# Kernel tuning notes

Hardware: AMD Instinct MI355X
Metric: run time of the kernel (lower is better)

The kernel has to match this reference:

```python
import jax, jax.numpy as jnp
import numpy as np

SEQ_LEN, BATCH, HID, ATT = 2048, 64, 512, 512


def setup_inputs() -> dict:
    key = jax.random.key(0)
    k1, k2, k3, k4, k5, k6 = jax.random.split(key, 6)
    return {
        "dec_out": jax.random.normal(k1, (BATCH, HID), dtype=jnp.float32),
        "enc_outs": jax.random.normal(k2, (SEQ_LEN, BATCH, HID), dtype=jnp.float32),
        "W_s": jax.random.normal(k3, (ATT, HID), dtype=jnp.float32) * (1.0 / np.sqrt(HID)),
        "W_t": jax.random.normal(k4, (ATT, HID), dtype=jnp.float32) * (1.0 / np.sqrt(HID)),
        "b_t": jax.random.normal(k5, (ATT,), dtype=jnp.float32) * 0.01,
        "v_a": jax.random.uniform(k6, (ATT,), dtype=jnp.float32, minval=-0.05, maxval=0.05),
    }


def reference(dec_out, enc_outs, W_s, W_t, b_t, v_a):
    # enc_att: (seq_len, batch, att) = W_s @ enc_outs
    enc_att = jnp.einsum('sbh,ah->sba', enc_outs, W_s)
    # dec_att: (batch, att) = W_t @ dec_out + b_t
    dec_att = dec_out @ W_t.T + b_t
    # score(b, s) = v_a . tanh(enc_att[s,b] + dec_att[b])
    scores = jnp.einsum('sba,a->bs', jnp.tanh(enc_att + dec_att[None, :, :]), v_a)
    return scores  # (batch, seq_len)
```

## Files before the change

kernel.cpp:

```cpp
#include <hip/hip_runtime.h>

typedef __attribute__((ext_vector_type(8))) short short8;
typedef __attribute__((ext_vector_type(4))) float f32x4;

#define SEQ 2048
#define BATCH 64
#define HID 512
#define ATT 512

__device__ __forceinline__ unsigned short f2bf(float f) {
  unsigned u = __float_as_uint(f);
  u += 0x7fffu + ((u >> 16) & 1u);
  return (unsigned short)(u >> 16);
}

__device__ __forceinline__ void dma16(const void* g, void* l) {
  __builtin_amdgcn_global_load_lds(
      (const __attribute__((address_space(1))) unsigned int*)g,
      (__attribute__((address_space(3))) unsigned int*)l, 16, 0, 0);
}

__global__ void bahdanau_pre(const float* __restrict__ dec_out,
                             const float* __restrict__ W_t,
                             const float* __restrict__ b_t,
                             const float* __restrict__ W_s,
                             unsigned short* __restrict__ wsb,
                             float* __restrict__ decT) {
  if (blockIdx.x < 64) {
    const int b = blockIdx.x;
    __shared__ float drow[HID];
    for (int i = threadIdx.x; i < HID; i += 256) drow[i] = dec_out[b * HID + i];
    __syncthreads();
    for (int a = threadIdx.x; a < ATT; a += 256) {
      const float4* wr = (const float4*)(W_t + (size_t)a * HID);
      float s0 = 0.f, s1 = 0.f, s2 = 0.f, s3 = 0.f;
#pragma unroll 4
      for (int j = 0; j < HID / 4; ++j) {
        float4 w = wr[j];
        s0 = fmaf(w.x, drow[4 * j + 0], s0);
        s1 = fmaf(w.y, drow[4 * j + 1], s1);
        s2 = fmaf(w.z, drow[4 * j + 2], s2);
        s3 = fmaf(w.w, drow[4 * j + 3], s3);
      }
      decT[a * BATCH + b] = (s0 + s1) + (s2 + s3) + b_t[a];
    }
  } else {
    const int cb = blockIdx.x - 64;
    const float4* src = (const float4*)W_s;
#pragma unroll
    for (int i = 0; i < 4; ++i) {
      int idx = cb * 1024 + i * 256 + threadIdx.x;
      float4 v = src[idx];
      int a = idx >> 7;
      int h = (idx & 127) * 4;
      ushort4 o;
      o.x = f2bf(v.x); o.y = f2bf(v.y); o.z = f2bf(v.z); o.w = f2bf(v.w);
      int blk = (a >> 4) * 64 + ((h >> 3) & 3) * 16 + (a & 15);
      int dst = (h >> 5) * 16384 + blk * 8 + (h & 7);
      *(ushort4*)&wsb[dst] = o;
    }
  }
}

__global__ __launch_bounds__(512, 2)
void bahdanau_main(const float* __restrict__ enc,
                   const unsigned short* __restrict__ wsb,
                   const float* __restrict__ decT,
                   const float* __restrict__ v_a,
                   float* __restrict__ out) {
  __shared__ __align__(16) unsigned char smem[81920];
  unsigned short* Bb[2] = { (unsigned short*)smem, (unsigned short*)(smem + 32768) };
  float* Ab[2] = { (float*)(smem + 65536), (float*)(smem + 73728) };
  float* partial = (float*)(smem + 65536);

  const int tid  = threadIdx.x;
  const int w    = tid >> 6;
  const int lane = tid & 63;
  const int c = lane & 15;
  const int q = lane >> 4;
  const int s = blockIdx.x;
  const int n0 = w * 64;

  const char* encB = (const char*)(enc + (size_t)s * 64 * HID);
  const char* wsbB = (const char*)wsb;

  const int am = (w & 3) * 16 + (lane & 15);
  const int ag = (lane >> 4) * 2 + (w >> 2);
  const char* aSrc = encB + am * 2048 + ag * 16;

  f32x4 acc[4][4];
#pragma unroll
  for (int nt = 0; nt < 4; ++nt)
#pragma unroll
    for (int mt = 0; mt < 4; ++mt)
      acc[mt][nt] = *(const f32x4*)(decT + (size_t)(n0 + nt * 16 + c) * 64 + mt * 16 + q * 4);

  float va[4];
#pragma unroll
  for (int nt = 0; nt < 4; ++nt) va[nt] = v_a[n0 + nt * 16 + c];

  dma16(aSrc, (char*)Ab[0] + w * 1024);
#pragma unroll
  for (int d = 0; d < 4; ++d)
    dma16(wsbB + w * 4096 + d * 1024 + lane * 16, (char*)Bb[0] + w * 4096 + d * 1024);

#pragma unroll
  for (int kb = 0; kb < 16; ++kb) {
    const int cur = kb & 1;
    __syncthreads();

    if (kb < 15) {
      const int nb = kb + 1;
      const int nxt = nb & 1;
      dma16(aSrc + nb * 128, (char*)Ab[nxt] + w * 1024);
#pragma unroll
      for (int d = 0; d < 4; ++d)
        dma16(wsbB + nb * 32768 + w * 4096 + d * 1024 + lane * 16,
              (char*)Bb[nxt] + w * 4096 + d * 1024);
    }

    const float* Ac = Ab[cur];
    const unsigned short* Bc = Bb[cur];
    short8 af[4];
#pragma unroll
    for (int mt = 0; mt < 4; ++mt) {
      float4 lo = *(const float4*)(Ac + (mt * 64 + q * 16 + c) * 4);
      float4 hi = *(const float4*)(Ac + (256 + mt * 64 + q * 16 + c) * 4);
      short8 t;
      t[0] = (short)f2bf(lo.x); t[1] = (short)f2bf(lo.y);
      t[2] = (short)f2bf(lo.z); t[3] = (short)f2bf(lo.w);
      t[4] = (short)f2bf(hi.x); t[5] = (short)f2bf(hi.y);
      t[6] = (short)f2bf(hi.z); t[7] = (short)f2bf(hi.w);
      af[mt] = t;
    }
    short8 bf[4];
#pragma unroll
    for (int nt = 0; nt < 4; ++nt)
      bf[nt] = *(const short8*)(Bc + (((w * 4 + nt) * 64 + q * 16 + c) * 8));

#pragma unroll
    for (int mt = 0; mt < 4; ++mt)
#pragma unroll
      for (int nt = 0; nt < 4; ++nt)
        acc[mt][nt] = __builtin_amdgcn_mfma_f32_16x16x32_bf16(af[mt], bf[nt], acc[mt][nt], 0, 0, 0);
  }

  float rowsum[4][4];
#pragma unroll
  for (int mt = 0; mt < 4; ++mt) {
#pragma unroll
    for (int r = 0; r < 4; ++r) {
      float sum = 0.f;
#pragma unroll
      for (int nt = 0; nt < 4; ++nt) {
        float x = acc[mt][nt][r];
        float e = __builtin_amdgcn_exp2f(x * 2.8853900817779268f);
        float t = 1.f - 2.f * __builtin_amdgcn_rcpf(e + 1.f);
        sum = fmaf(va[nt], t, sum);
      }
      rowsum[mt][r] = sum;
    }
  }

#pragma unroll
  for (int off = 1; off < 16; off <<= 1) {
#pragma unroll
    for (int mt = 0; mt < 4; ++mt)
#pragma unroll
      for (int r = 0; r < 4; ++r)
        rowsum[mt][r] += __shfl_xor(rowsum[mt][r], off, 64);
  }

  if (c == 0) {
#pragma unroll
    for (int mt = 0; mt < 4; ++mt)
#pragma unroll
      for (int r = 0; r < 4; ++r)
        partial[w * 64 + mt * 16 + q * 4 + r] = rowsum[mt][r];
  }
  __syncthreads();

  if (tid < 64) {
    float sum = 0.f;
#pragma unroll
    for (int ww = 0; ww < 8; ++ww) sum += partial[ww * 64 + tid];
    out[(size_t)tid * SEQ + s] = sum;
  }
}

extern "C" void kernel_launch(void* const* d_in, const int* in_sizes, int n_in,
                              void* d_out, int out_size, void* d_ws, size_t ws_size,
                              hipStream_t stream) {
  const float* dec_out = (const float*)d_in[0];
  const float* enc     = (const float*)d_in[1];
  const float* W_s     = (const float*)d_in[2];
  const float* W_t     = (const float*)d_in[3];
  const float* b_t     = (const float*)d_in[4];
  const float* v_a     = (const float*)d_in[5];
  float* out = (float*)d_out;

  unsigned short* wsb = (unsigned short*)d_ws;
  float* decT = (float*)((char*)d_ws + (size_t)ATT * HID * 2);

  bahdanau_pre<<<128, 256, 0, stream>>>(dec_out, W_t, b_t, W_s, wsb, decT);
  bahdanau_main<<<SEQ, 512, 0, stream>>>(enc, wsb, decT, v_a, out);
}
```

Baseline: 489.4 us.

## Load W_s fragments directly to registers and deepen A-tile pipeline

```diff
diff --git a/kernel.cpp b/kernel.cpp
--- a/kernel.cpp
+++ b/kernel.cpp
@@ -19,6 +19,23 @@
       (const __attribute__((address_space(1))) unsigned int*)g,
       (__attribute__((address_space(3))) unsigned int*)l, 16, 0, 0);
 }
+
+__device__ __forceinline__ short8 cvt8(float4 lo, float4 hi) {
+  union { unsigned u[4]; short8 s; } r;
+  asm("v_cvt_pk_bf16_f32 %0, %1, %2" : "=v"(r.u[0]) : "v"(lo.x), "v"(lo.y));
+  asm("v_cvt_pk_bf16_f32 %0, %1, %2" : "=v"(r.u[1]) : "v"(lo.z), "v"(lo.w));
+  asm("v_cvt_pk_bf16_f32 %0, %1, %2" : "=v"(r.u[2]) : "v"(hi.x), "v"(hi.y));
+  asm("v_cvt_pk_bf16_f32 %0, %1, %2" : "=v"(r.u[3]) : "v"(hi.z), "v"(hi.w));
+  return r.s;
+}
+
+#define GLOADS(dst, voff, base, OFF) \
+  asm volatile("global_load_dwordx4 %0, %1, %2 offset:" #OFF \
+               : "=v"(dst) : "v"(voff), "s"(base))
+
+#define BWAIT(N, b0, b1, b2, b3) \
+  asm volatile("s_waitcnt vmcnt(" #N ")" \
+               : "+v"(b0), "+v"(b1), "+v"(b2), "+v"(b3) :: "memory")
 
 __global__ void bahdanau_pre(const float* __restrict__ dec_out,
                              const float* __restrict__ W_t,
@@ -62,16 +79,14 @@
   }
 }
 
-__global__ __launch_bounds__(512, 2)
+__global__ __launch_bounds__(512, 4)
 void bahdanau_main(const float* __restrict__ enc,
                    const unsigned short* __restrict__ wsb,
                    const float* __restrict__ decT,
                    const float* __restrict__ v_a,
                    float* __restrict__ out) {
-  __shared__ __align__(16) unsigned char smem[81920];
-  unsigned short* Bb[2] = { (unsigned short*)smem, (unsigned short*)(smem + 32768) };
-  float* Ab[2] = { (float*)(smem + 65536), (float*)(smem + 73728) };
-  float* partial = (float*)(smem + 65536);
+  __shared__ __align__(16) float Asm[4][2048];
+  __shared__ float partial[512];
 
   const int tid  = threadIdx.x;
   const int w    = tid >> 6;
@@ -82,11 +97,12 @@
   const int n0 = w * 64;
 
   const char* encB = (const char*)(enc + (size_t)s * 64 * HID);
-  const char* wsbB = (const char*)wsb;
-
-  const int am = (w & 3) * 16 + (lane & 15);
-  const int ag = (lane >> 4) * 2 + (w >> 2);
+
+  const int am = (w & 3) * 16 + c;
+  const int ag = q * 2 + (w >> 2);
   const char* aSrc = encB + am * 2048 + ag * 16;
+
+  const unsigned voff = (unsigned)(w * 256 + q * 16 + c) * 16u;
 
   f32x4 acc[4][4];
 #pragma unroll
@@ -95,55 +111,50 @@
     for (int mt = 0; mt < 4; ++mt)
       acc[mt][nt] = *(const f32x4*)(decT + (size_t)(n0 + nt * 16 + c) * 64 + mt * 16 + q * 4);
 
-  float va[4];
-#pragma unroll
-  for (int nt = 0; nt < 4; ++nt) va[nt] = v_a[n0 + nt * 16 + c];
-
-  dma16(aSrc, (char*)Ab[0] + w * 1024);
-#pragma unroll
-  for (int d = 0; d < 4; ++d)
-    dma16(wsbB + w * 4096 + d * 1024 + lane * 16, (char*)Bb[0] + w * 4096 + d * 1024);
+  asm volatile("s_waitcnt vmcnt(0)" ::: "memory");
+
+  short8 bf[2][4];
+
+  dma16(aSrc, &Asm[0][w * 256]);
+  GLOADS(bf[0][0], voff, wsb, 0);
+  GLOADS(bf[0][1], voff, wsb, 1024);
+  GLOADS(bf[0][2], voff, wsb, 2048);
+  GLOADS(bf[0][3], voff, wsb, 3072);
+  dma16(aSrc + 128, &Asm[1][w * 256]);
 
 #pragma unroll
   for (int kb = 0; kb < 16; ++kb) {
-    const int cur = kb & 1;
-    __syncthreads();
-
-    if (kb < 15) {
-      const int nb = kb + 1;
-      const int nxt = nb & 1;
-      dma16(aSrc + nb * 128, (char*)Ab[nxt] + w * 1024);
-#pragma unroll
-      for (int d = 0; d < 4; ++d)
-        dma16(wsbB + nb * 32768 + w * 4096 + d * 1024 + lane * 16,
-              (char*)Bb[nxt] + w * 4096 + d * 1024);
-    }
-
-    const float* Ac = Ab[cur];
-    const unsigned short* Bc = Bb[cur];
-    short8 af[4];
+    if (kb + 1 < 16) {
+      const unsigned short* bk = wsb + (size_t)(kb + 1) * 16384;
+      GLOADS(bf[(kb + 1) & 1][0], voff, bk, 0);
+      GLOADS(bf[(kb + 1) & 1][1], voff, bk, 1024);
+      GLOADS(bf[(kb + 1) & 1][2], voff, bk, 2048);
+      GLOADS(bf[(kb + 1) & 1][3], voff, bk, 3072);
+    }
+    if (kb + 2 < 16)
+      dma16(aSrc + (kb + 2) * 128, &Asm[(kb + 2) & 3][w * 256]);
+
+    if (kb <= 13)      BWAIT(6, bf[kb & 1][0], bf[kb & 1][1], bf[kb & 1][2], bf[kb & 1][3]);
+    else if (kb == 14) BWAIT(5, bf[kb & 1][0], bf[kb & 1][1], bf[kb & 1][2], bf[kb & 1][3]);
+    else               BWAIT(0, bf[kb & 1][0], bf[kb & 1][1], bf[kb & 1][2], bf[kb & 1][3]);
+    __builtin_amdgcn_s_barrier();
+
+    const float* Ac = &Asm[kb & 3][0];
 #pragma unroll
     for (int mt = 0; mt < 4; ++mt) {
       float4 lo = *(const float4*)(Ac + (mt * 64 + q * 16 + c) * 4);
       float4 hi = *(const float4*)(Ac + (256 + mt * 64 + q * 16 + c) * 4);
-      short8 t;
-      t[0] = (short)f2bf(lo.x); t[1] = (short)f2bf(lo.y);
-      t[2] = (short)f2bf(lo.z); t[3] = (short)f2bf(lo.w);
-      t[4] = (short)f2bf(hi.x); t[5] = (short)f2bf(hi.y);
-      t[6] = (short)f2bf(hi.z); t[7] = (short)f2bf(hi.w);
-      af[mt] = t;
-    }
-    short8 bf[4];
-#pragma unroll
-    for (int nt = 0; nt < 4; ++nt)
-      bf[nt] = *(const short8*)(Bc + (((w * 4 + nt) * 64 + q * 16 + c) * 8));
-
-#pragma unroll
-    for (int mt = 0; mt < 4; ++mt)
+      short8 af = cvt8(lo, hi);
 #pragma unroll
       for (int nt = 0; nt < 4; ++nt)
-        acc[mt][nt] = __builtin_amdgcn_mfma_f32_16x16x32_bf16(af[mt], bf[nt], acc[mt][nt], 0, 0, 0);
-  }
+        acc[mt][nt] = __builtin_amdgcn_mfma_f32_16x16x32_bf16(af, bf[kb & 1][nt], acc[mt][nt], 0, 0, 0);
+    }
+    asm volatile("s_waitcnt lgkmcnt(0)" ::: "memory");
+  }
+
+  float va[4];
+#pragma unroll
+  for (int nt = 0; nt < 4; ++nt) va[nt] = v_a[n0 + nt * 16 + c];
 
   float rowsum[4][4];
 #pragma unroll
```

Result: no change. 482.4 us (-1.4%).
